# Kernel tuning notes

Hardware: AMD Instinct MI355X
Metric: run time of the kernel (lower is better)

The kernel has to match this reference:

```python
import jax, jax.numpy as jnp
import numpy as np

E = 8          # num_experts
H = 2048       # hidden_size
D = 4096       # expert_dim
R = 8          # lora rank
SCALE = 16.0 / 8.0  # lora_alpha / r
T = 2048       # tokens per expert


def setup_inputs() -> dict:
    key = jax.random.key(0)
    ks = jax.random.split(key, 7)
    s = lambda *shape: 1.0 / np.sqrt(shape[-1])
    hidden_states = jax.random.normal(ks[0], (E * T, H), dtype=jnp.float32)
    # base weights (nn.Linear convention: [out, in]) stacked over experts
    W_gu = jax.random.normal(ks[1], (E, 2 * D, H), dtype=jnp.float32) * s(H)
    W_d = jax.random.normal(ks[2], (E, H, D), dtype=jnp.float32) * s(D)
    # LoRA factors: A [r, in] (kaiming-ish), B [out, r] (zeros in training init;
    # use small random here so the delta path is exercised)
    A_gu = jax.random.normal(ks[3], (E, R, H), dtype=jnp.float32) * s(H)
    B_gu = jax.random.normal(ks[4], (E, 2 * D, R), dtype=jnp.float32) * 0.01
    A_d = jax.random.normal(ks[5], (E, R, D), dtype=jnp.float32) * s(D)
    B_d = jax.random.normal(ks[6], (E, H, R), dtype=jnp.float32) * 0.01
    return {"hidden_states": hidden_states, "W_gu": W_gu, "A_gu": A_gu,
            "B_gu": B_gu, "W_d": W_d, "A_d": A_d, "B_d": B_d}


def _lora_linear(x, W, A, B):
    # x: [e, t, in]; W: [e, out, in]; A: [e, r, in]; B: [e, out, r]
    base = jnp.einsum('eti,eoi->eto', x, W)
    low = jnp.einsum('eti,eri->etr', x, A)        # skinny projection
    delta = jnp.einsum('etr,eor->eto', low, B)
    return base + SCALE * delta


def reference(hidden_states, W_gu, A_gu, B_gu, W_d, A_d, B_d):
    x = hidden_states.reshape(E, -1, H)           # [E, T, H]
    gate_up = _lora_linear(x, W_gu, A_gu, B_gu)   # [E, T, 2D]
    gate, up = gate_up[..., :D], gate_up[..., D:]
    h = up * jax.nn.silu(gate)                    # SwiGLU [E, T, D]
    out = _lora_linear(h, W_d, A_d, B_d)          # [E, T, H]
    return out.reshape(-1, H)
```

## Files before the change

kernel.cpp:

```cpp
#include <hip/hip_runtime.h>
#include <hip/hip_bf16.h>

#define E_ 8
#define H_ 2048
#define D_ 4096
#define R_ 8
#define T_ 2048
#define TWO_D_ 8192
#define SCALE_ 2.0f

typedef __attribute__((ext_vector_type(8))) short short8;
typedef __attribute__((ext_vector_type(4))) float f32x4;

__device__ __forceinline__ unsigned short f2bf(float f) {
  union { float f; unsigned u; } c; c.f = f;
  unsigned u = c.u + 0x7fffu + ((c.u >> 16) & 1u);
  return (unsigned short)(u >> 16);
}
__device__ __forceinline__ float bf2f(unsigned short s) {
  union { unsigned u; float f; } c; c.u = ((unsigned)s) << 16;
  return c.f;
}

__device__ __forceinline__ void gl16(const void* g, void* l) {
  __builtin_amdgcn_global_load_lds(
      (const __attribute__((address_space(1))) void*)g,
      (__attribute__((address_space(3))) void*)l, 16, 0, 0);
}

__device__ __forceinline__ int lds_off(int rr, int ks, int lq) {
  return (((rr >> 5) & 3) << 13) | (((rr >> 7) & 1) << 12) | ((rr & 31) << 7) | (ks << 6) | (lq << 4);
}

__global__ __launch_bounds__(256) void k_pre(const float* __restrict__ x,
                                             const float* __restrict__ Agu,
                                             float* __restrict__ low,
                                             unsigned short* __restrict__ xb,
                                             const float* __restrict__ Wgu,
                                             unsigned short* __restrict__ wgub,
                                             const float* __restrict__ Wd,
                                             unsigned short* __restrict__ wdb) {
  const int NB_LOW = E_ * T_ / 4;
  if (blockIdx.x < NB_LOW) {
    int wave = (blockIdx.x * 256 + threadIdx.x) >> 6;
    int lane = threadIdx.x & 63;
    int e = wave >> 11;
    const float* Ae = Agu + (long)e * R_ * H_;
    float acc[R_] = {0.f,0.f,0.f,0.f,0.f,0.f,0.f,0.f};
    for (int it = 0; it < H_ / 256; ++it) {
      int i = it * 256 + lane * 4;
      const float* xp = x + (long)wave * H_;
      f32x4 v = *(const f32x4*)(xp + i);
      ushort4 u; u.x=f2bf(v[0]); u.y=f2bf(v[1]); u.z=f2bf(v[2]); u.w=f2bf(v[3]);
      *(ushort4*)(xb + (long)wave * H_ + i) = u;
      #pragma unroll
      for (int r = 0; r < R_; ++r) {
        f32x4 a = *(const f32x4*)(Ae + r * H_ + i);
        acc[r] += v[0]*a[0] + v[1]*a[1] + v[2]*a[2] + v[3]*a[3];
      }
    }
    #pragma unroll
    for (int r = 0; r < R_; ++r) {
      float v = acc[r];
      #pragma unroll
      for (int off = 32; off > 0; off >>= 1) v += __shfl_xor(v, off);
      acc[r] = v;
    }
    if (lane == 0) {
      #pragma unroll
      for (int r = 0; r < R_; ++r) low[(long)wave * R_ + r] = acc[r];
    }
  } else if (blockIdx.x < NB_LOW + 1024) {
    const long n = (long)E_ * TWO_D_ * H_;
    long i = ((long)(blockIdx.x - NB_LOW) * 256 + threadIdx.x) * 8;
    const long stride = (long)1024 * 256 * 8;
    for (; i < n; i += stride) {
      f32x4 a = *(const f32x4*)(Wgu + i);
      f32x4 b = *(const f32x4*)(Wgu + i + 4);
      ushort4 lo, hi;
      lo.x=f2bf(a[0]); lo.y=f2bf(a[1]); lo.z=f2bf(a[2]); lo.w=f2bf(a[3]);
      hi.x=f2bf(b[0]); hi.y=f2bf(b[1]); hi.z=f2bf(b[2]); hi.w=f2bf(b[3]);
      *(ushort4*)(wgub + i) = lo;
      *(ushort4*)(wgub + i + 4) = hi;
    }
  } else {
    const long n = (long)E_ * H_ * D_;
    long i = ((long)(blockIdx.x - NB_LOW - 1024) * 256 + threadIdx.x) * 8;
    const long stride = (long)1024 * 256 * 8;
    for (; i < n; i += stride) {
      f32x4 a = *(const f32x4*)(Wd + i);
      f32x4 b = *(const f32x4*)(Wd + i + 4);
      ushort4 lo, hi;
      lo.x=f2bf(a[0]); lo.y=f2bf(a[1]); lo.z=f2bf(a[2]); lo.w=f2bf(a[3]);
      hi.x=f2bf(b[0]); hi.y=f2bf(b[1]); hi.z=f2bf(b[2]); hi.w=f2bf(b[3]);
      *(ushort4*)(wdb + i) = lo;
      *(ushort4*)(wdb + i + 4) = hi;
    }
  }
}

__global__ __launch_bounds__(256) void k_low2(const unsigned short* __restrict__ Hb,
                                              const float* __restrict__ Ad,
                                              float* __restrict__ low) {
  int wave = (blockIdx.x * 256 + threadIdx.x) >> 6;
  int lane = threadIdx.x & 63;
  int e = wave >> 11;
  const float* Ae = Ad + (long)e * R_ * D_;
  float acc[R_] = {0.f,0.f,0.f,0.f,0.f,0.f,0.f,0.f};
  for (int it = 0; it < D_ / 256; ++it) {
    int i = it * 256 + lane * 4;
    ushort4 u = *(const ushort4*)(Hb + (long)wave * D_ + i);
    float xv[4] = {bf2f(u.x), bf2f(u.y), bf2f(u.z), bf2f(u.w)};
    #pragma unroll
    for (int r = 0; r < R_; ++r) {
      f32x4 a = *(const f32x4*)(Ae + r * D_ + i);
      acc[r] += xv[0]*a[0] + xv[1]*a[1] + xv[2]*a[2] + xv[3]*a[3];
    }
  }
  #pragma unroll
  for (int r = 0; r < R_; ++r) {
    float v = acc[r];
    #pragma unroll
    for (int off = 32; off > 0; off >>= 1) v += __shfl_xor(v, off);
    acc[r] = v;
  }
  if (lane == 0) {
    #pragma unroll
    for (int r = 0; r < R_; ++r) low[(long)wave * R_ + r] = acc[r];
  }
}

__global__ __launch_bounds__(512, 2) void k_gemm1_8p(
    const unsigned short* __restrict__ Xb, const unsigned short* __restrict__ Wb,
    const float* __restrict__ Bgu, const float* __restrict__ low,
    unsigned short* __restrict__ Hout) {
  __shared__ __align__(16) char lds[131072];

  const int MT = T_ / 256, NT = D_ / 128;
  int b = blockIdx.x;
  int cpx = (int)gridDim.x >> 3;
  int swz = (b & 7) * cpx + (b >> 3);
  int e  = swz / (MT * NT);
  int r0 = swz % (MT * NT);
  int nt = r0 / MT, mt = r0 % MT;

  int tid = threadIdx.x, lane = tid & 63;
  int wid = tid >> 6, wm = wid >> 2, wn = wid & 3;
  int lrow = lane & 15, lq = lane >> 4;
  int X4 = (lrow & 7) << 4;
  const int NKT = H_ / 64;

  unsigned ro = (unsigned)tid * 16;
  unsigned so = ro ^ (((ro >> 7) & 7u) << 4);
  int sh = (so >> 12) & 1, sr = (so >> 7) & 31, sc = (so & 127) >> 1;
  const unsigned short* pA[4]; const unsigned short* pB[4];
  #pragma unroll
  for (int q = 0; q < 4; ++q) {
    long arow = (long)e * T_ + mt * 256 + sh * 128 + q * 32 + sr;
    pA[q] = Xb + arow * H_ + sc;
    long wrow = sh ? ((long)e * TWO_D_ + D_ + nt * 128 + q * 32 + sr)
                   : ((long)e * TWO_D_ +      nt * 128 + q * 32 + sr);
    pB[q] = Wb + wrow * (long)H_ + sc;
  }
  auto SA = [&](int d, int q) { gl16(pA[q], lds + d * 32768 + q * 8192 + ro); pA[q] += 64; };
  auto SB = [&](int d, int q) { gl16(pB[q], lds + 65536 + d * 32768 + q * 8192 + ro); pB[q] += 64; };

  f32x4 accg[2][8] = {}, accu[2][8] = {};
  short8 BG[2][2], BU[2][2], af[2][2];

  SA(0,0); SB(0,0); SA(0,1); SB(0,1); SA(0,2); SB(0,2); SA(0,3); SB(0,3);
  SA(1,0); SB(1,0); SA(1,1); SB(1,1); SA(1,2); SB(1,2);
  asm volatile("s_waitcnt vmcnt(6)" ::: "memory");
  __builtin_amdgcn_s_barrier();

  int rbA = wm * 128 + lrow;
  for (int t = 0; t < NKT; ++t) {
    int d = t & 1;
    const char* Ab = lds + d * 32768;
    const char* Bb = lds + 65536 + d * 32768;

#define G1_MFMA(q)                                                                   \
    __builtin_amdgcn_s_setprio(1);                                                   \
    _Pragma("unroll") for (int m2 = 0; m2 < 2; ++m2)                                 \
      _Pragma("unroll") for (int ks = 0; ks < 2; ++ks)                               \
        _Pragma("unroll") for (int nj = 0; nj < 2; ++nj) {                           \
          accg[nj][(q)*2+m2] = __builtin_amdgcn_mfma_f32_16x16x32_bf16(              \
              BG[nj][ks], af[m2][ks], accg[nj][(q)*2+m2], 0, 0, 0);                  \
          accu[nj][(q)*2+m2] = __builtin_amdgcn_mfma_f32_16x16x32_bf16(              \
              BU[nj][ks], af[m2][ks], accu[nj][(q)*2+m2], 0, 0, 0);                  \
        }                                                                            \
    __builtin_amdgcn_s_setprio(0);

#define G1_LDA(q)                                                                    \
    _Pragma("unroll") for (int m2 = 0; m2 < 2; ++m2)                                 \
      _Pragma("unroll") for (int ks = 0; ks < 2; ++ks)                               \
        af[m2][ks] = *(const short8*)(Ab + (lds_off(rbA + ((q)*2+m2)*16, ks, lq) ^ X4));

#define G1_SYNC()                                                                    \
    __builtin_amdgcn_s_barrier();                                                    \
    asm volatile("s_waitcnt lgkmcnt(0)" ::: "memory");                               \
    __builtin_amdgcn_sched_barrier(0);

    #pragma unroll
    for (int nj = 0; nj < 2; ++nj)
      #pragma unroll
      for (int ks = 0; ks < 2; ++ks) {
        int rg = wn * 32 + nj * 16 + lrow;
        BG[nj][ks] = *(const short8*)(Bb + (lds_off(rg, ks, lq) ^ X4));
        BU[nj][ks] = *(const short8*)(Bb + (lds_off(rg + 128, ks, lq) ^ X4));
      }
    G1_LDA(0);
    if (t + 1 < NKT) { SA(d ^ 1, 3); SB(d ^ 1, 3); }
    G1_SYNC();
    G1_MFMA(0);
    __builtin_amdgcn_s_barrier();
    G1_LDA(1);
    if (t + 2 < NKT) { SA(d, 0); SB(d, 0); }
    G1_SYNC();
    G1_MFMA(1);
    __builtin_amdgcn_s_barrier();
    G1_LDA(2);
    if (t + 2 < NKT) { SA(d, 1); SB(d, 1); }
    G1_SYNC();
    G1_MFMA(2);
    __builtin_amdgcn_s_barrier();
    G1_LDA(3);
    if (t + 2 < NKT) {
      SA(d, 2); SB(d, 2);
      asm volatile("s_waitcnt vmcnt(6)" ::: "memory");
    } else {
      asm volatile("s_waitcnt vmcnt(0)" ::: "memory");
    }
    G1_SYNC();
    G1_MFMA(3);
    __builtin_amdgcn_s_barrier();
  }

  __syncthreads();
  unsigned short* sLo2 = (unsigned short*)lds;
  unsigned short* sB2  = (unsigned short*)(lds + 16384);
  {
    short8 z = {};
    if (tid < 256) {
      const float* lp = low + ((long)e * T_ + mt * 256 + tid) * R_;
      short8 v;
      #pragma unroll
      for (int r = 0; r < 8; ++r) ((unsigned short*)&v)[r] = f2bf(SCALE_ * lp[r]);
      *(short8*)(sLo2 + tid * 32) = v;
      *(short8*)(sLo2 + tid * 32 + 8) = z;
      *(short8*)(sLo2 + tid * 32 + 16) = z;
      *(short8*)(sLo2 + tid * 32 + 24) = z;
    } else {
      int r = tid - 256;
      long wrow = (r < 128) ? ((long)e * TWO_D_ + nt * 128 + r)
                            : ((long)e * TWO_D_ + D_ + nt * 128 + (r - 128));
      const float* bp = Bgu + wrow * R_;
      short8 v;
      #pragma unroll
      for (int k = 0; k < 8; ++k) ((unsigned short*)&v)[k] = f2bf(bp[k]);
      *(short8*)(sB2 + r * 32) = v;
      *(short8*)(sB2 + r * 32 + 8) = z;
      *(short8*)(sB2 + r * 32 + 16) = z;
      *(short8*)(sB2 + r * 32 + 24) = z;
    }
  }
  __syncthreads();
  {
    #pragma unroll
    for (int mi = 0; mi < 8; ++mi) {
      short8 alo = *(const short8*)(sLo2 + (rbA + mi * 16) * 32 + lq * 8);
      #pragma unroll
      for (int nj = 0; nj < 2; ++nj) {
        int rg = wn * 32 + nj * 16 + lrow;
        short8 bg2 = *(const short8*)(sB2 + rg * 32 + lq * 8);
        short8 bu2 = *(const short8*)(sB2 + (rg + 128) * 32 + lq * 8);
        accg[nj][mi] = __builtin_amdgcn_mfma_f32_16x16x32_bf16(bg2, alo, accg[nj][mi], 0, 0, 0);
        accu[nj][mi] = __builtin_amdgcn_mfma_f32_16x16x32_bf16(bu2, alo, accu[nj][mi], 0, 0, 0);
      }
    }
  }
  unsigned short* sT = (unsigned short*)(lds + 32768);
  #pragma unroll
  for (int mi = 0; mi < 8; ++mi) {
    int tl = rbA + mi * 16;
    #pragma unroll
    for (int nj = 0; nj < 2; ++nj) {
      int cb = wn * 32 + nj * 16 + lq * 4;
      ushort4 o;
      #pragma unroll
      for (int j = 0; j < 4; ++j) {
        float gate = accg[nj][mi][j];
        float up   = accu[nj][mi][j];
        float hh = up * (gate / (1.f + __expf(-gate)));
        (&o.x)[j] = f2bf(hh);
      }
      *(ushort4*)(sT + tl * 136 + cb) = o;
    }
  }
  __syncthreads();
  {
    long base = ((long)e * T_ + mt * 256) * D_ + nt * 128;
    int rr2 = tid >> 4, cc2 = (tid & 15) * 8;
    #pragma unroll
    for (int p = 0; p < 8; ++p) {
      int r = p * 32 + rr2;
      short8 v = *(const short8*)(sT + r * 136 + cc2);
      *(short8*)(Hout + base + (long)r * D_ + cc2) = v;
    }
  }
}

__global__ __launch_bounds__(512, 2) void k_gemm2_8p(
    const unsigned short* __restrict__ Hin, const unsigned short* __restrict__ Wdb,
    const float* __restrict__ Bd, const float* __restrict__ low,
    float* __restrict__ Out) {
  __shared__ __align__(16) char lds[131072];

  const int MT = T_ / 256, NT = H_ / 256;
  int b = blockIdx.x;
  int cpx = (int)gridDim.x >> 3;
  int swz = (b & 7) * cpx + (b >> 3);
  int e  = swz / (MT * NT);
  int r0 = swz % (MT * NT);
  int nt = r0 / MT, mt = r0 % MT;

  int tid = threadIdx.x, lane = tid & 63;
  int wid = tid >> 6, wm = wid >> 2, wn = wid & 3;
  int lrow = lane & 15, lq = lane >> 4;
  int X4 = (lrow & 7) << 4;
  const int NKT = D_ / 64;

  unsigned ro = (unsigned)tid * 16;
  unsigned so = ro ^ (((ro >> 7) & 7u) << 4);
  int sh = (so >> 12) & 1, sr = (so >> 7) & 31, sc = (so & 127) >> 1;
  const unsigned short* pA[4]; const unsigned short* pB[4];
  #pragma unroll
  for (int q = 0; q < 4; ++q) {
    long arow = (long)e * T_ + mt * 256 + sh * 128 + q * 32 + sr;
    pA[q] = Hin + arow * D_ + sc;
    long wrow = (long)e * H_ + nt * 256 + sh * 128 + q * 32 + sr;
    pB[q] = Wdb + wrow * (long)D_ + sc;
  }
  auto SA = [&](int d, int q) { gl16(pA[q], lds + d * 32768 + q * 8192 + ro); pA[q] += 64; };
  auto SB = [&](int d, int q) { gl16(pB[q], lds + 65536 + d * 32768 + q * 8192 + ro); pB[q] += 64; };

  f32x4 acc[8][4] = {};
  short8 BF[4][2], af[2][2];

  SA(0,0); SB(0,0); SA(0,1); SB(0,1); SA(0,2); SB(0,2); SA(0,3); SB(0,3);
  SA(1,0); SB(1,0); SA(1,1); SB(1,1); SA(1,2); SB(1,2);
  asm volatile("s_waitcnt vmcnt(6)" ::: "memory");
  __builtin_amdgcn_s_barrier();

  int rbA = wm * 128 + lrow;
  for (int t = 0; t < NKT; ++t) {
    int d = t & 1;
    const char* Ab = lds + d * 32768;
    const char* Bb = lds + 65536 + d * 32768;

#define G2_MFMA(q)                                                                   \
    __builtin_amdgcn_s_setprio(1);                                                   \
    _Pragma("unroll") for (int m2 = 0; m2 < 2; ++m2)                                 \
      _Pragma("unroll") for (int ks = 0; ks < 2; ++ks)                               \
        _Pragma("unroll") for (int ni = 0; ni < 4; ++ni)                             \
          acc[(q)*2+m2][ni] = __builtin_amdgcn_mfma_f32_16x16x32_bf16(               \
              af[m2][ks], BF[ni][ks], acc[(q)*2+m2][ni], 0, 0, 0);                   \
    __builtin_amdgcn_s_setprio(0);

#define G2_LDA(q)                                                                    \
    _Pragma("unroll") for (int m2 = 0; m2 < 2; ++m2)                                 \
      _Pragma("unroll") for (int ks = 0; ks < 2; ++ks)                               \
        af[m2][ks] = *(const short8*)(Ab + (lds_off(rbA + ((q)*2+m2)*16, ks, lq) ^ X4));

    #pragma unroll
    for (int ni = 0; ni < 4; ++ni)
      #pragma unroll
      for (int ks = 0; ks < 2; ++ks)
        BF[ni][ks] = *(const short8*)(Bb + (lds_off(wn * 64 + ni * 16 + lrow, ks, lq) ^ X4));
    G2_LDA(0);
    if (t + 1 < NKT) { SA(d ^ 1, 3); SB(d ^ 1, 3); }
    __builtin_amdgcn_s_barrier();
    asm volatile("s_waitcnt lgkmcnt(0)" ::: "memory");
    __builtin_amdgcn_sched_barrier(0);
    G2_MFMA(0);
    __builtin_amdgcn_s_barrier();
    G2_LDA(1);
    if (t + 2 < NKT) { SA(d, 0); SB(d, 0); }
    __builtin_amdgcn_s_barrier();
    asm volatile("s_waitcnt lgkmcnt(0)" ::: "memory");
    __builtin_amdgcn_sched_barrier(0);
    G2_MFMA(1);
    __builtin_amdgcn_s_barrier();
    G2_LDA(2);
    if (t + 2 < NKT) { SA(d, 1); SB(d, 1); }
    __builtin_amdgcn_s_barrier();
    asm volatile("s_waitcnt lgkmcnt(0)" ::: "memory");
    __builtin_amdgcn_sched_barrier(0);
    G2_MFMA(2);
    __builtin_amdgcn_s_barrier();
    G2_LDA(3);
    if (t + 2 < NKT) {
      SA(d, 2); SB(d, 2);
      asm volatile("s_waitcnt vmcnt(6)" ::: "memory");
    } else {
      asm volatile("s_waitcnt vmcnt(0)" ::: "memory");
    }
    __builtin_amdgcn_s_barrier();
    asm volatile("s_waitcnt lgkmcnt(0)" ::: "memory");
    __builtin_amdgcn_sched_barrier(0);
    G2_MFMA(3);
    __builtin_amdgcn_s_barrier();
  }

  __syncthreads();
  unsigned short* sLo2 = (unsigned short*)lds;
  unsigned short* sB2  = (unsigned short*)(lds + 16384);
  {
    short8 z = {};
    if (tid < 256) {
      const float* lp = low + ((long)e * T_ + mt * 256 + tid) * R_;
      short8 v;
      #pragma unroll
      for (int r = 0; r < 8; ++r) ((unsigned short*)&v)[r] = f2bf(SCALE_ * lp[r]);
      *(short8*)(sLo2 + tid * 32) = v;
      *(short8*)(sLo2 + tid * 32 + 8) = z;
      *(short8*)(sLo2 + tid * 32 + 16) = z;
      *(short8*)(sLo2 + tid * 32 + 24) = z;
    } else {
      int r = tid - 256;
      const float* bp = Bd + ((long)e * H_ + nt * 256 + r) * R_;
      short8 v;
      #pragma unroll
      for (int k = 0; k < 8; ++k) ((unsigned short*)&v)[k] = f2bf(bp[k]);
      *(short8*)(sB2 + r * 32) = v;
      *(short8*)(sB2 + r * 32 + 8) = z;
      *(short8*)(sB2 + r * 32 + 16) = z;
      *(short8*)(sB2 + r * 32 + 24) = z;
    }
  }
  __syncthreads();
  #pragma unroll
  for (int mi = 0; mi < 8; ++mi) {
    short8 alo = *(const short8*)(sLo2 + (rbA + mi * 16) * 32 + lq * 8);
    #pragma unroll
    for (int ni = 0; ni < 4; ++ni) {
      short8 bd2 = *(const short8*)(sB2 + (wn * 64 + ni * 16 + lrow) * 32 + lq * 8);
      acc[mi][ni] = __builtin_amdgcn_mfma_f32_16x16x32_bf16(alo, bd2, acc[mi][ni], 0, 0, 0);
    }
  }
  {
    long rowbase = (long)e * T_ + mt * 256 + wm * 128;
    int colbase = nt * 256 + wn * 64;
    #pragma unroll
    for (int mi = 0; mi < 8; ++mi)
      #pragma unroll
      for (int j = 0; j < 4; ++j) {
        long row = rowbase + mi * 16 + lq * 4 + j;
        #pragma unroll
        for (int ni = 0; ni < 4; ++ni)
          Out[row * H_ + colbase + ni * 16 + lrow] = acc[mi][ni][j];
      }
  }
}

extern "C" void kernel_launch(void* const* d_in, const int* in_sizes, int n_in,
                              void* d_out, int out_size, void* d_ws, size_t ws_size,
                              hipStream_t stream) {
  const float* x   = (const float*)d_in[0];
  const float* Wgu = (const float*)d_in[1];
  const float* Agu = (const float*)d_in[2];
  const float* Bgu = (const float*)d_in[3];
  const float* Wd  = (const float*)d_in[4];
  const float* Ad  = (const float*)d_in[5];
  const float* Bd  = (const float*)d_in[6];
  float* out = (float*)d_out;

  char* ws = (char*)d_ws;
  const size_t SZ_H   = (size_t)E_ * T_ * D_ * 2;
  const size_t SZ_LOW = (size_t)E_ * T_ * R_ * 4;
  const size_t SZ_XB  = (size_t)E_ * T_ * H_ * 2;
  const size_t SZ_WGU = (size_t)E_ * TWO_D_ * H_ * 2;

  unsigned short* hbuf = (unsigned short*)ws;
  float* low1 = (float*)(ws + SZ_H);
  float* low2 = (float*)(ws + SZ_H + SZ_LOW);
  unsigned short* xb   = (unsigned short*)(ws + SZ_H + 2 * SZ_LOW);
  unsigned short* wgub = (unsigned short*)(ws + SZ_H + 2 * SZ_LOW + SZ_XB);
  unsigned short* wdb  = (unsigned short*)(ws + SZ_H + 2 * SZ_LOW + SZ_XB + SZ_WGU);

  hipLaunchKernelGGL(k_pre, dim3(E_ * T_ / 4 + 2048), dim3(256), 0, stream,
                     x, Agu, low1, xb, Wgu, wgub, Wd, wdb);
  hipLaunchKernelGGL(k_gemm1_8p, dim3(E_ * (T_ / 256) * (D_ / 128)), dim3(512), 0, stream,
                     xb, wgub, Bgu, low1, hbuf);
  hipLaunchKernelGGL(k_low2, dim3(E_ * T_ / 4), dim3(256), 0, stream, hbuf, Ad, low2);
  hipLaunchKernelGGL(k_gemm2_8p, dim3(E_ * (T_ / 256) * (H_ / 256)), dim3(512), 0, stream,
                     hbuf, wdb, Bd, low2, out);
}
```

Baseline: 1.125 ms.

## Replace interleaved 4-phase K-loop with whole-tile LDS read then bulk prefetch

Both GEMM main loops drop the four-phase schedule, which interleaved LDS fragment reads, global-to-LDS prefetches and barriers per quarter tile. Each iteration now reads all A and B fragments for the K-tile into registers, runs every MFMA, then issues the full next-next tile prefetch with one wait. The goal is to cut per-iteration barriers and waitcnt stalls, at the cost of more live fragment registers and less overlap of global loads with MFMA work.

```diff
diff --git a/kernel.cpp b/kernel.cpp
--- a/kernel.cpp
+++ b/kernel.cpp
@@ -166,11 +166,10 @@
   auto SB = [&](int d, int q) { gl16(pB[q], lds + 65536 + d * 32768 + q * 8192 + ro); pB[q] += 64; };
 
   f32x4 accg[2][8] = {}, accu[2][8] = {};
-  short8 BG[2][2], BU[2][2], af[2][2];
 
   SA(0,0); SB(0,0); SA(0,1); SB(0,1); SA(0,2); SB(0,2); SA(0,3); SB(0,3);
-  SA(1,0); SB(1,0); SA(1,1); SB(1,1); SA(1,2); SB(1,2);
-  asm volatile("s_waitcnt vmcnt(6)" ::: "memory");
+  SA(1,0); SB(1,0); SA(1,1); SB(1,1); SA(1,2); SB(1,2); SA(1,3); SB(1,3);
+  asm volatile("s_waitcnt vmcnt(8)" ::: "memory");
   __builtin_amdgcn_s_barrier();
 
   int rbA = wm * 128 + lrow;
@@ -179,28 +178,7 @@
     const char* Ab = lds + d * 32768;
     const char* Bb = lds + 65536 + d * 32768;
 
-#define G1_MFMA(q)                                                                   \
-    __builtin_amdgcn_s_setprio(1);                                                   \
-    _Pragma("unroll") for (int m2 = 0; m2 < 2; ++m2)                                 \
-      _Pragma("unroll") for (int ks = 0; ks < 2; ++ks)                               \
-        _Pragma("unroll") for (int nj = 0; nj < 2; ++nj) {                           \
-          accg[nj][(q)*2+m2] = __builtin_amdgcn_mfma_f32_16x16x32_bf16(              \
-              BG[nj][ks], af[m2][ks], accg[nj][(q)*2+m2], 0, 0, 0);                  \
-          accu[nj][(q)*2+m2] = __builtin_amdgcn_mfma_f32_16x16x32_bf16(              \
-              BU[nj][ks], af[m2][ks], accu[nj][(q)*2+m2], 0, 0, 0);                  \
-        }                                                                            \
-    __builtin_amdgcn_s_setprio(0);
-
-#define G1_LDA(q)                                                                    \
-    _Pragma("unroll") for (int m2 = 0; m2 < 2; ++m2)                                 \
-      _Pragma("unroll") for (int ks = 0; ks < 2; ++ks)                               \
-        af[m2][ks] = *(const short8*)(Ab + (lds_off(rbA + ((q)*2+m2)*16, ks, lq) ^ X4));
-
-#define G1_SYNC()                                                                    \
-    __builtin_amdgcn_s_barrier();                                                    \
-    asm volatile("s_waitcnt lgkmcnt(0)" ::: "memory");                               \
-    __builtin_amdgcn_sched_barrier(0);
-
+    short8 BG[2][2], BU[2][2], af[4][2][2];
     #pragma unroll
     for (int nj = 0; nj < 2; ++nj)
       #pragma unroll
@@ -209,30 +187,38 @@
         BG[nj][ks] = *(const short8*)(Bb + (lds_off(rg, ks, lq) ^ X4));
         BU[nj][ks] = *(const short8*)(Bb + (lds_off(rg + 128, ks, lq) ^ X4));
       }
-    G1_LDA(0);
-    if (t + 1 < NKT) { SA(d ^ 1, 3); SB(d ^ 1, 3); }
-    G1_SYNC();
-    G1_MFMA(0);
+    #pragma unroll
+    for (int q = 0; q < 4; ++q)
+      #pragma unroll
+      for (int m2 = 0; m2 < 2; ++m2)
+        #pragma unroll
+        for (int ks = 0; ks < 2; ++ks)
+          af[q][m2][ks] = *(const short8*)(Ab + (lds_off(rbA + (q * 2 + m2) * 16, ks, lq) ^ X4));
+
+    __builtin_amdgcn_s_setprio(1);
+    #pragma unroll
+    for (int q = 0; q < 4; ++q)
+      #pragma unroll
+      for (int m2 = 0; m2 < 2; ++m2)
+        #pragma unroll
+        for (int ks = 0; ks < 2; ++ks)
+          #pragma unroll
+          for (int nj = 0; nj < 2; ++nj) {
+            accg[nj][q*2+m2] = __builtin_amdgcn_mfma_f32_16x16x32_bf16(
+                BG[nj][ks], af[q][m2][ks], accg[nj][q*2+m2], 0, 0, 0);
+            accu[nj][q*2+m2] = __builtin_amdgcn_mfma_f32_16x16x32_bf16(
+                BU[nj][ks], af[q][m2][ks], accu[nj][q*2+m2], 0, 0, 0);
+          }
+    __builtin_amdgcn_s_setprio(0);
+
     __builtin_amdgcn_s_barrier();
-    G1_LDA(1);
-    if (t + 2 < NKT) { SA(d, 0); SB(d, 0); }
-    G1_SYNC();
-    G1_MFMA(1);
-    __builtin_amdgcn_s_barrier();
-    G1_LDA(2);
-    if (t + 2 < NKT) { SA(d, 1); SB(d, 1); }
-    G1_SYNC();
-    G1_MFMA(2);
-    __builtin_amdgcn_s_barrier();
-    G1_LDA(3);
+    __builtin_amdgcn_sched_barrier(0);
     if (t + 2 < NKT) {
-      SA(d, 2); SB(d, 2);
-      asm volatile("s_waitcnt vmcnt(6)" ::: "memory");
+      SA(d,0); SB(d,0); SA(d,1); SB(d,1); SA(d,2); SB(d,2); SA(d,3); SB(d,3);
+      asm volatile("s_waitcnt vmcnt(8)" ::: "memory");
     } else {
       asm volatile("s_waitcnt vmcnt(0)" ::: "memory");
     }
-    G1_SYNC();
-    G1_MFMA(3);
     __builtin_amdgcn_s_barrier();
   }
 
@@ -345,11 +331,10 @@
   auto SB = [&](int d, int q) { gl16(pB[q], lds + 65536 + d * 32768 + q * 8192 + ro); pB[q] += 64; };
 
   f32x4 acc[8][4] = {};
-  short8 BF[4][2], af[2][2];
 
   SA(0,0); SB(0,0); SA(0,1); SB(0,1); SA(0,2); SB(0,2); SA(0,3); SB(0,3);
-  SA(1,0); SB(1,0); SA(1,1); SB(1,1); SA(1,2); SB(1,2);
-  asm volatile("s_waitcnt vmcnt(6)" ::: "memory");
+  SA(1,0); SB(1,0); SA(1,1); SB(1,1); SA(1,2); SB(1,2); SA(1,3); SB(1,3);
+  asm volatile("s_waitcnt vmcnt(8)" ::: "memory");
   __builtin_amdgcn_s_barrier();
 
   int rbA = wm * 128 + lrow;
@@ -358,57 +343,41 @@
     const char* Ab = lds + d * 32768;
     const char* Bb = lds + 65536 + d * 32768;
 
-#define G2_MFMA(q)                                                                   \
-    __builtin_amdgcn_s_setprio(1);                                                   \
-    _Pragma("unroll") for (int m2 = 0; m2 < 2; ++m2)                                 \
-      _Pragma("unroll") for (int ks = 0; ks < 2; ++ks)                               \
-        _Pragma("unroll") for (int ni = 0; ni < 4; ++ni)                             \
-          acc[(q)*2+m2][ni] = __builtin_amdgcn_mfma_f32_16x16x32_bf16(               \
-              af[m2][ks], BF[ni][ks], acc[(q)*2+m2][ni], 0, 0, 0);                   \
-    __builtin_amdgcn_s_setprio(0);
-
-#define G2_LDA(q)                                                                    \
-    _Pragma("unroll") for (int m2 = 0; m2 < 2; ++m2)                                 \
-      _Pragma("unroll") for (int ks = 0; ks < 2; ++ks)                               \
-        af[m2][ks] = *(const short8*)(Ab + (lds_off(rbA + ((q)*2+m2)*16, ks, lq) ^ X4));
-
+    short8 BF[4][2], af[4][2][2];
     #pragma unroll
     for (int ni = 0; ni < 4; ++ni)
       #pragma unroll
       for (int ks = 0; ks < 2; ++ks)
         BF[ni][ks] = *(const short8*)(Bb + (lds_off(wn * 64 + ni * 16 + lrow, ks, lq) ^ X4));
-    G2_LDA(0);
-    if (t + 1 < NKT) { SA(d ^ 1, 3); SB(d ^ 1, 3); }
+    #pragma unroll
+    for (int q = 0; q < 4; ++q)
+      #pragma unroll
+      for (int m2 = 0; m2 < 2; ++m2)
+        #pragma unroll
+        for (int ks = 0; ks < 2; ++ks)
+          af[q][m2][ks] = *(const short8*)(Ab + (lds_off(rbA + (q * 2 + m2) * 16, ks, lq) ^ X4));
+
+    __builtin_amdgcn_s_setprio(1);
+    #pragma unroll
+    for (int q = 0; q < 4; ++q)
+      #pragma unroll
+      for (int m2 = 0; m2 < 2; ++m2)
+        #pragma unroll
+        for (int ks = 0; ks < 2; ++ks)
+          #pragma unroll
+          for (int ni = 0; ni < 4; ++ni)
+            acc[q*2+m2][ni] = __builtin_amdgcn_mfma_f32_16x16x32_bf16(
+                af[q][m2][ks], BF[ni][ks], acc[q*2+m2][ni], 0, 0, 0);
+    __builtin_amdgcn_s_setprio(0);
+
     __builtin_amdgcn_s_barrier();
-    asm volatile("s_waitcnt lgkmcnt(0)" ::: "memory");
     __builtin_amdgcn_sched_barrier(0);
-    G2_MFMA(0);
-    __builtin_amdgcn_s_barrier();
-    G2_LDA(1);
-    if (t + 2 < NKT) { SA(d, 0); SB(d, 0); }
-    __builtin_amdgcn_s_barrier();
-    asm volatile("s_waitcnt lgkmcnt(0)" ::: "memory");
-    __builtin_amdgcn_sched_barrier(0);
-    G2_MFMA(1);
-    __builtin_amdgcn_s_barrier();
-    G2_LDA(2);
-    if (t + 2 < NKT) { SA(d, 1); SB(d, 1); }
-    __builtin_amdgcn_s_barrier();
-    asm volatile("s_waitcnt lgkmcnt(0)" ::: "memory");
-    __builtin_amdgcn_sched_barrier(0);
-    G2_MFMA(2);
-    __builtin_amdgcn_s_barrier();
-    G2_LDA(3);
     if (t + 2 < NKT) {
-      SA(d, 2); SB(d, 2);
-      asm volatile("s_waitcnt vmcnt(6)" ::: "memory");
+      SA(d,0); SB(d,0); SA(d,1); SB(d,1); SA(d,2); SB(d,2); SA(d,3); SB(d,3);
+      asm volatile("s_waitcnt vmcnt(8)" ::: "memory");
     } else {
       asm volatile("s_waitcnt vmcnt(0)" ::: "memory");
     }
-    __builtin_amdgcn_s_barrier();
-    asm volatile("s_waitcnt lgkmcnt(0)" ::: "memory");
-    __builtin_amdgcn_sched_barrier(0);
-    G2_MFMA(3);
     __builtin_amdgcn_s_barrier();
   }
 
```

Result: slower. 1.592 ms (+41.6%).

## Fuse second LoRA down-projection into gemm1 epilogue with atomic accumulation

Applied to the files above, without the earlier changes.

Removes the separate k_low2 kernel, which re-read the whole bf16 intermediate H from global memory. Instead, the gemm1 epilogue multiplies its 256x128 SwiGLU tile, already staged in LDS, by the matching A_d slice and atomically adds partial rank-8 sums into low2. A memset of low2 is added beforehand. This trades a full pass over H for extra epilogue work, 32 atomics per token per row, and results that can vary with float atomic ordering.

```diff
diff --git a/kernel.cpp b/kernel.cpp
--- a/kernel.cpp
+++ b/kernel.cpp
@@ -99,41 +99,11 @@
   }
 }
 
-__global__ __launch_bounds__(256) void k_low2(const unsigned short* __restrict__ Hb,
-                                              const float* __restrict__ Ad,
-                                              float* __restrict__ low) {
-  int wave = (blockIdx.x * 256 + threadIdx.x) >> 6;
-  int lane = threadIdx.x & 63;
-  int e = wave >> 11;
-  const float* Ae = Ad + (long)e * R_ * D_;
-  float acc[R_] = {0.f,0.f,0.f,0.f,0.f,0.f,0.f,0.f};
-  for (int it = 0; it < D_ / 256; ++it) {
-    int i = it * 256 + lane * 4;
-    ushort4 u = *(const ushort4*)(Hb + (long)wave * D_ + i);
-    float xv[4] = {bf2f(u.x), bf2f(u.y), bf2f(u.z), bf2f(u.w)};
-    #pragma unroll
-    for (int r = 0; r < R_; ++r) {
-      f32x4 a = *(const f32x4*)(Ae + r * D_ + i);
-      acc[r] += xv[0]*a[0] + xv[1]*a[1] + xv[2]*a[2] + xv[3]*a[3];
-    }
-  }
-  #pragma unroll
-  for (int r = 0; r < R_; ++r) {
-    float v = acc[r];
-    #pragma unroll
-    for (int off = 32; off > 0; off >>= 1) v += __shfl_xor(v, off);
-    acc[r] = v;
-  }
-  if (lane == 0) {
-    #pragma unroll
-    for (int r = 0; r < R_; ++r) low[(long)wave * R_ + r] = acc[r];
-  }
-}
-
 __global__ __launch_bounds__(512, 2) void k_gemm1_8p(
     const unsigned short* __restrict__ Xb, const unsigned short* __restrict__ Wb,
     const float* __restrict__ Bgu, const float* __restrict__ low,
-    unsigned short* __restrict__ Hout) {
+    unsigned short* __restrict__ Hout,
+    const float* __restrict__ Ad, float* __restrict__ low2out) {
   __shared__ __align__(16) char lds[131072];
 
   const int MT = T_ / 256, NT = D_ / 128;
@@ -239,6 +209,7 @@
   __syncthreads();
   unsigned short* sLo2 = (unsigned short*)lds;
   unsigned short* sB2  = (unsigned short*)(lds + 16384);
+  float* sAd = (float*)(lds + 102400);
   {
     short8 z = {};
     if (tid < 256) {
@@ -263,6 +234,13 @@
       *(short8*)(sB2 + r * 32 + 16) = z;
       *(short8*)(sB2 + r * 32 + 24) = z;
     }
+    {
+      int idx = tid * 2;
+      int r = idx >> 7, c = idx & 127;
+      const float* ap = Ad + ((long)e * R_ + r) * D_ + nt * 128 + c;
+      sAd[r * 128 + c] = ap[0];
+      sAd[r * 128 + c + 1] = ap[1];
+    }
   }
   __syncthreads();
   {
@@ -306,6 +284,30 @@
       int r = p * 32 + rr2;
       short8 v = *(const short8*)(sT + r * 136 + cc2);
       *(short8*)(Hout + base + (long)r * D_ + cc2) = v;
+    }
+  }
+  {
+    int tl = wid * 32 + (lane & 31);
+    int c0 = (lane >> 5) * 64;
+    float sums[8] = {0.f,0.f,0.f,0.f,0.f,0.f,0.f,0.f};
+    #pragma unroll
+    for (int ch = 0; ch < 8; ++ch) {
+      short8 hv = *(const short8*)(sT + tl * 136 + c0 + ch * 8);
+      float hf[8];
+      #pragma unroll
+      for (int j = 0; j < 8; ++j) hf[j] = bf2f(((unsigned short*)&hv)[j]);
+      #pragma unroll
+      for (int r = 0; r < 8; ++r) {
+        const float* ap = sAd + r * 128 + c0 + ch * 8;
+        #pragma unroll
+        for (int j = 0; j < 8; ++j) sums[r] += hf[j] * ap[j];
+      }
+    }
+    long tok = (long)e * T_ + mt * 256 + tl;
+    #pragma unroll
+    for (int r = 0; r < 8; ++r) {
+      float v = sums[r] + __shfl_xor(sums[r], 32);
+      if ((lane >> 5) == 0) atomicAdd(&low2out[tok * R_ + r], v);
     }
   }
 }
@@ -488,11 +490,11 @@
   unsigned short* wgub = (unsigned short*)(ws + SZ_H + 2 * SZ_LOW + SZ_XB);
   unsigned short* wdb  = (unsigned short*)(ws + SZ_H + 2 * SZ_LOW + SZ_XB + SZ_WGU);
 
+  hipMemsetAsync(low2, 0, SZ_LOW, stream);
   hipLaunchKernelGGL(k_pre, dim3(E_ * T_ / 4 + 2048), dim3(256), 0, stream,
                      x, Agu, low1, xb, Wgu, wgub, Wd, wdb);
   hipLaunchKernelGGL(k_gemm1_8p, dim3(E_ * (T_ / 256) * (D_ / 128)), dim3(512), 0, stream,
-                     xb, wgub, Bgu, low1, hbuf);
-  hipLaunchKernelGGL(k_low2, dim3(E_ * T_ / 4), dim3(256), 0, stream, hbuf, Ad, low2);
+                     xb, wgub, Bgu, low1, hbuf, Ad, low2);
   hipLaunchKernelGGL(k_gemm2_8p, dim3(E_ * (T_ / 256) * (H_ / 256)), dim3(512), 0, stream,
                      hbuf, wdb, Bd, low2, out);
 }
```

Result: slower. 1.491 ms (+32.5%).

## Double-buffer LDS-to-register fragments so reads overlap MFMA in both GEMMs

Applied to the files above, without the earlier changes.

Both GEMM main loops now keep two sets of A and B register fragments. The next quarter's (or next k-tile's) LDS reads are issued before the current MFMA block runs, and the explicit lgkmcnt(0) waits before each MFMA block are removed, so LDS latency can hide behind matrix math. The loop is unrolled by two k-tiles to alternate the B fragment buffers. This raises register pressure, which may cut occupancy. It also depends on barrier placement staying correct, since some LDS waits are now left to the compiler.

```diff
diff --git a/kernel.cpp b/kernel.cpp
--- a/kernel.cpp
+++ b/kernel.cpp
@@ -166,74 +166,83 @@
   auto SB = [&](int d, int q) { gl16(pB[q], lds + 65536 + d * 32768 + q * 8192 + ro); pB[q] += 64; };
 
   f32x4 accg[2][8] = {}, accu[2][8] = {};
-  short8 BG[2][2], BU[2][2], af[2][2];
-
-  SA(0,0); SB(0,0); SA(0,1); SB(0,1); SA(0,2); SB(0,2); SA(0,3); SB(0,3);
-  SA(1,0); SB(1,0); SA(1,1); SB(1,1); SA(1,2); SB(1,2);
-  asm volatile("s_waitcnt vmcnt(6)" ::: "memory");
-  __builtin_amdgcn_s_barrier();
-
+  short8 af0[2][2], af1[2][2];
+  short8 BGa[2][2], BUa[2][2], BGb[2][2], BUb[2][2];
   int rbA = wm * 128 + lrow;
-  for (int t = 0; t < NKT; ++t) {
-    int d = t & 1;
-    const char* Ab = lds + d * 32768;
-    const char* Bb = lds + 65536 + d * 32768;
-
-#define G1_MFMA(q)                                                                   \
+
+#define G1_MFMA(q, AF, BGs, BUs)                                                     \
     __builtin_amdgcn_s_setprio(1);                                                   \
     _Pragma("unroll") for (int m2 = 0; m2 < 2; ++m2)                                 \
       _Pragma("unroll") for (int ks = 0; ks < 2; ++ks)                               \
         _Pragma("unroll") for (int nj = 0; nj < 2; ++nj) {                           \
           accg[nj][(q)*2+m2] = __builtin_amdgcn_mfma_f32_16x16x32_bf16(              \
-              BG[nj][ks], af[m2][ks], accg[nj][(q)*2+m2], 0, 0, 0);                  \
+              BGs[nj][ks], AF[m2][ks], accg[nj][(q)*2+m2], 0, 0, 0);                 \
           accu[nj][(q)*2+m2] = __builtin_amdgcn_mfma_f32_16x16x32_bf16(              \
-              BU[nj][ks], af[m2][ks], accu[nj][(q)*2+m2], 0, 0, 0);                  \
+              BUs[nj][ks], AF[m2][ks], accu[nj][(q)*2+m2], 0, 0, 0);                 \
         }                                                                            \
     __builtin_amdgcn_s_setprio(0);
 
-#define G1_LDA(q)                                                                    \
+#define G1_LDA_Q(AF, Ab, q)                                                          \
     _Pragma("unroll") for (int m2 = 0; m2 < 2; ++m2)                                 \
       _Pragma("unroll") for (int ks = 0; ks < 2; ++ks)                               \
-        af[m2][ks] = *(const short8*)(Ab + (lds_off(rbA + ((q)*2+m2)*16, ks, lq) ^ X4));
-
-#define G1_SYNC()                                                                    \
-    __builtin_amdgcn_s_barrier();                                                    \
-    asm volatile("s_waitcnt lgkmcnt(0)" ::: "memory");                               \
-    __builtin_amdgcn_sched_barrier(0);
-
-    #pragma unroll
-    for (int nj = 0; nj < 2; ++nj)
-      #pragma unroll
-      for (int ks = 0; ks < 2; ++ks) {
-        int rg = wn * 32 + nj * 16 + lrow;
-        BG[nj][ks] = *(const short8*)(Bb + (lds_off(rg, ks, lq) ^ X4));
-        BU[nj][ks] = *(const short8*)(Bb + (lds_off(rg + 128, ks, lq) ^ X4));
+        AF[m2][ks] = *(const short8*)((Ab) + (lds_off(rbA + ((q)*2+m2)*16, ks, lq) ^ X4));
+
+#define G1_LDB(BGs, BUs, Bb)                                                         \
+    _Pragma("unroll") for (int nj = 0; nj < 2; ++nj)                                 \
+      _Pragma("unroll") for (int ks = 0; ks < 2; ++ks) {                             \
+        int rg = wn * 32 + nj * 16 + lrow;                                           \
+        BGs[nj][ks] = *(const short8*)((Bb) + (lds_off(rg, ks, lq) ^ X4));           \
+        BUs[nj][ks] = *(const short8*)((Bb) + (lds_off(rg + 128, ks, lq) ^ X4));     \
       }
-    G1_LDA(0);
-    if (t + 1 < NKT) { SA(d ^ 1, 3); SB(d ^ 1, 3); }
-    G1_SYNC();
-    G1_MFMA(0);
-    __builtin_amdgcn_s_barrier();
-    G1_LDA(1);
-    if (t + 2 < NKT) { SA(d, 0); SB(d, 0); }
-    G1_SYNC();
-    G1_MFMA(1);
-    __builtin_amdgcn_s_barrier();
-    G1_LDA(2);
-    if (t + 2 < NKT) { SA(d, 1); SB(d, 1); }
-    G1_SYNC();
-    G1_MFMA(2);
-    __builtin_amdgcn_s_barrier();
-    G1_LDA(3);
-    if (t + 2 < NKT) {
-      SA(d, 2); SB(d, 2);
-      asm volatile("s_waitcnt vmcnt(6)" ::: "memory");
-    } else {
-      asm volatile("s_waitcnt vmcnt(0)" ::: "memory");
-    }
-    G1_SYNC();
-    G1_MFMA(3);
-    __builtin_amdgcn_s_barrier();
+
+#define G1_TILE(tt, BGc, BUc, BGn, BUn)                                              \
+  {                                                                                  \
+    int d = (tt) & 1;                                                                \
+    const char* Ab  = lds + d * 32768;                                               \
+    const char* AbN = lds + (d ^ 1) * 32768;                                         \
+    const char* BbN = lds + 65536 + (d ^ 1) * 32768;                                 \
+                                                                        \
+    if ((tt) + 1 < NKT) { SA(d ^ 1, 3); SB(d ^ 1, 3); }                              \
+    G1_LDA_Q(af1, Ab, 1);                                                            \
+    __builtin_amdgcn_sched_barrier(0);                                               \
+    G1_MFMA(0, af0, BGc, BUc);                                                       \
+    __builtin_amdgcn_s_barrier();                                                    \
+                                                                        \
+    if ((tt) + 2 < NKT) { SA(d, 0); SB(d, 0); }                                      \
+    G1_LDA_Q(af0, Ab, 2);                                                            \
+    __builtin_amdgcn_sched_barrier(0);                                               \
+    G1_MFMA(1, af1, BGc, BUc);                                                       \
+    __builtin_amdgcn_s_barrier();                                                    \
+                                                                        \
+    if ((tt) + 2 < NKT) { SA(d, 1); SB(d, 1); }                                      \
+    G1_LDA_Q(af1, Ab, 3);                                                            \
+    __builtin_amdgcn_sched_barrier(0);                                               \
+    G1_MFMA(2, af0, BGc, BUc);                                                       \
+    __builtin_amdgcn_s_barrier();                                                    \
+           \
+    if ((tt) + 2 < NKT) {                                                            \
+      SA(d, 2); SB(d, 2);                                                            \
+      asm volatile("s_waitcnt vmcnt(6)" ::: "memory");                               \
+    } else {                                                                         \
+      asm volatile("s_waitcnt vmcnt(0)" ::: "memory");                               \
+    }                                                                                \
+    __builtin_amdgcn_s_barrier();                                                    \
+    if ((tt) + 1 < NKT) { G1_LDB(BGn, BUn, BbN); G1_LDA_Q(af0, AbN, 0); }            \
+    __builtin_amdgcn_sched_barrier(0);                                               \
+    G1_MFMA(3, af1, BGc, BUc);                                                       \
+    __builtin_amdgcn_s_barrier();                                                    \
+  }
+
+  SA(0,0); SB(0,0); SA(0,1); SB(0,1); SA(0,2); SB(0,2); SA(0,3); SB(0,3);
+  SA(1,0); SB(1,0); SA(1,1); SB(1,1); SA(1,2); SB(1,2);
+  asm volatile("s_waitcnt vmcnt(6)" ::: "memory");
+  __builtin_amdgcn_s_barrier();
+  G1_LDB(BGa, BUa, lds + 65536);
+  G1_LDA_Q(af0, lds, 0);
+
+  for (int t = 0; t < NKT; t += 2) {
+    G1_TILE(t,     BGa, BUa, BGb, BUb);
+    G1_TILE(t + 1, BGb, BUb, BGa, BUa);
   }
 
   __syncthreads();
@@ -345,71 +354,77 @@
   auto SB = [&](int d, int q) { gl16(pB[q], lds + 65536 + d * 32768 + q * 8192 + ro); pB[q] += 64; };
 
   f32x4 acc[8][4] = {};
-  short8 BF[4][2], af[2][2];
-
-  SA(0,0); SB(0,0); SA(0,1); SB(0,1); SA(0,2); SB(0,2); SA(0,3); SB(0,3);
-  SA(1,0); SB(1,0); SA(1,1); SB(1,1); SA(1,2); SB(1,2);
-  asm volatile("s_waitcnt vmcnt(6)" ::: "memory");
-  __builtin_amdgcn_s_barrier();
-
+  short8 af0[2][2], af1[2][2];
+  short8 BFa[4][2], BFb[4][2];
   int rbA = wm * 128 + lrow;
-  for (int t = 0; t < NKT; ++t) {
-    int d = t & 1;
-    const char* Ab = lds + d * 32768;
-    const char* Bb = lds + 65536 + d * 32768;
-
-#define G2_MFMA(q)                                                                   \
+
+#define G2_MFMA(q, AF, BFs)                                                          \
     __builtin_amdgcn_s_setprio(1);                                                   \
     _Pragma("unroll") for (int m2 = 0; m2 < 2; ++m2)                                 \
       _Pragma("unroll") for (int ks = 0; ks < 2; ++ks)                               \
         _Pragma("unroll") for (int ni = 0; ni < 4; ++ni)                             \
           acc[(q)*2+m2][ni] = __builtin_amdgcn_mfma_f32_16x16x32_bf16(               \
-              af[m2][ks], BF[ni][ks], acc[(q)*2+m2][ni], 0, 0, 0);                   \
+              AF[m2][ks], BFs[ni][ks], acc[(q)*2+m2][ni], 0, 0, 0);                  \
     __builtin_amdgcn_s_setprio(0);
 
-#define G2_LDA(q)                                                                    \
+#define G2_LDA_Q(AF, Ab, q)                                                          \
     _Pragma("unroll") for (int m2 = 0; m2 < 2; ++m2)                                 \
       _Pragma("unroll") for (int ks = 0; ks < 2; ++ks)                               \
-        af[m2][ks] = *(const short8*)(Ab + (lds_off(rbA + ((q)*2+m2)*16, ks, lq) ^ X4));
-
-    #pragma unroll
-    for (int ni = 0; ni < 4; ++ni)
-      #pragma unroll
-      for (int ks = 0; ks < 2; ++ks)
-        BF[ni][ks] = *(const short8*)(Bb + (lds_off(wn * 64 + ni * 16 + lrow, ks, lq) ^ X4));
-    G2_LDA(0);
-    if (t + 1 < NKT) { SA(d ^ 1, 3); SB(d ^ 1, 3); }
-    __builtin_amdgcn_s_barrier();
-    asm volatile("s_waitcnt lgkmcnt(0)" ::: "memory");
-    __builtin_amdgcn_sched_barrier(0);
-    G2_MFMA(0);
-    __builtin_amdgcn_s_barrier();
-    G2_LDA(1);
-    if (t + 2 < NKT) { SA(d, 0); SB(d, 0); }
-    __builtin_amdgcn_s_barrier();
-    asm volatile("s_waitcnt lgkmcnt(0)" ::: "memory");
-    __builtin_amdgcn_sched_barrier(0);
-    G2_MFMA(1);
-    __builtin_amdgcn_s_barrier();
-    G2_LDA(2);
-    if (t + 2 < NKT) { SA(d, 1); SB(d, 1); }
-    __builtin_amdgcn_s_barrier();
-    asm volatile("s_waitcnt lgkmcnt(0)" ::: "memory");
-    __builtin_amdgcn_sched_barrier(0);
-    G2_MFMA(2);
-    __builtin_amdgcn_s_barrier();
-    G2_LDA(3);
-    if (t + 2 < NKT) {
-      SA(d, 2); SB(d, 2);
-      asm volatile("s_waitcnt vmcnt(6)" ::: "memory");
-    } else {
-      asm volatile("s_waitcnt vmcnt(0)" ::: "memory");
-    }
-    __builtin_amdgcn_s_barrier();
-    asm volatile("s_waitcnt lgkmcnt(0)" ::: "memory");
-    __builtin_amdgcn_sched_barrier(0);
-    G2_MFMA(3);
-    __builtin_amdgcn_s_barrier();
+        AF[m2][ks] = *(const short8*)((Ab) + (lds_off(rbA + ((q)*2+m2)*16, ks, lq) ^ X4));
+
+#define G2_LDB(BFs, Bb)                                                              \
+    _Pragma("unroll") for (int ni = 0; ni < 4; ++ni)                                 \
+      _Pragma("unroll") for (int ks = 0; ks < 2; ++ks)                               \
+        BFs[ni][ks] = *(const short8*)((Bb) + (lds_off(wn * 64 + ni * 16 + lrow, ks, lq) ^ X4));
+
+#define G2_TILE(tt, BFc, BFn)                                                        \
+  {                                                                                  \
+    int d = (tt) & 1;                                                                \
+    const char* Ab  = lds + d * 32768;                                               \
+    const char* AbN = lds + (d ^ 1) * 32768;                                         \
+    const char* BbN = lds + 65536 + (d ^ 1) * 32768;                                 \
+                                                                        \
+    if ((tt) + 1 < NKT) { SA(d ^ 1, 3); SB(d ^ 1, 3); }                              \
+    G2_LDA_Q(af1, Ab, 1);                                                            \
+    __builtin_amdgcn_sched_barrier(0);                                               \
+    G2_MFMA(0, af0, BFc);                                                            \
+    __builtin_amdgcn_s_barrier();                                                    \
+                                                                        \
+    if ((tt) + 2 < NKT) { SA(d, 0); SB(d, 0); }                                      \
+    G2_LDA_Q(af0, Ab, 2);                                                            \
+    __builtin_amdgcn_sched_barrier(0);                                               \
+    G2_MFMA(1, af1, BFc);                                                            \
+    __builtin_amdgcn_s_barrier();                                                    \
+                                                                        \
+    if ((tt) + 2 < NKT) { SA(d, 1); SB(d, 1); }                                      \
+    G2_LDA_Q(af1, Ab, 3);                                                            \
+    __builtin_amdgcn_sched_barrier(0);                                               \
+    G2_MFMA(2, af0, BFc);                                                            \
+    __builtin_amdgcn_s_barrier();                                                    \
+                                                                        \
+    if ((tt) + 2 < NKT) {                                                            \
+      SA(d, 2); SB(d, 2);                                                            \
+      asm volatile("s_waitcnt vmcnt(6)" ::: "memory");                               \
+    } else {                                                                         \
+      asm volatile("s_waitcnt vmcnt(0)" ::: "memory");                               \
+    }                                                                                \
+    __builtin_amdgcn_s_barrier();                                                    \
+    if ((tt) + 1 < NKT) { G2_LDB(BFn, BbN); G2_LDA_Q(af0, AbN, 0); }                 \
+    __builtin_amdgcn_sched_barrier(0);                                               \
+    G2_MFMA(3, af1, BFc);                                                            \
+    __builtin_amdgcn_s_barrier();                                                    \
+  }
+
+  SA(0,0); SB(0,0); SA(0,1); SB(0,1); SA(0,2); SB(0,2); SA(0,3); SB(0,3);
+  SA(1,0); SB(1,0); SA(1,1); SB(1,1); SA(1,2); SB(1,2);
+  asm volatile("s_waitcnt vmcnt(6)" ::: "memory");
+  __builtin_amdgcn_s_barrier();
+  G2_LDB(BFa, lds + 65536);
+  G2_LDA_Q(af0, lds, 0);
+
+  for (int t = 0; t < NKT; t += 2) {
+    G2_TILE(t,     BFa, BFb);
+    G2_TILE(t + 1, BFb, BFa);
   }
 
   __syncthreads();
```

New measurement: 3.249 ms. +188.8%, slower.
